# Performance work log

Measured on AMD Instinct MI355X. Metric: run time of the kernel, lower is better.

Reference implementation:

```python
import jax, jax.numpy as jnp
import numpy as np

E = 1024      # embed_dim
QH = 16       # query heads
KVH = 4       # kv heads
HD = E // QH  # head_dim = 64
KVE = HD * KVH  # 256
EPS = 1e-5
ROPE_BASE = 10000.0


def rope(x, d):
    # Faithful to the source RoPE: d == number of heads (x.shape[-2]),
    # and the 'sequence' axis of the cache is x.shape[0] (the batch dim).
    # rope(x) = x*cos + (x*sin) * neg_half(x)  (note: nonlinear in x).
    b = x.shape[0]
    theta = 1.0 / (ROPE_BASE ** (jnp.arange(0, d, 2, dtype=jnp.float32) / d))  # (d//2,)
    seq_idx = jnp.arange(b, dtype=jnp.float32)                                 # (b,)
    idx_theta = seq_idx[:, None] * theta[None, :]                              # (b, d//2)
    idx2 = jnp.concatenate([idx_theta, idx_theta], axis=-1)                    # (b, d)
    # cached shape (b,1,1,d); source permutes (0,1,3,2) -> (b,1,d,1)
    cos = jnp.cos(idx2)[:, None, :, None]  # (b,1,d,1)
    sin = jnp.sin(idx2)[:, None, :, None]
    d2 = d // 2
    # split of the LAST dim (head_dim) at d//2 == num_heads//2, as in source
    neg = jnp.concatenate([-x[..., d2:], x[..., :d2]], axis=-1)
    return x * cos + (x * sin) * neg


def setup_inputs() -> dict:
    key = jax.random.key(0)
    ks = jax.random.split(key, 12)
    b, n = 1, 2048

    def xavier(k, shape):
        fan_out, fan_in = shape
        std = (2.0 / (fan_in + fan_out)) ** 0.5
        return jax.random.normal(k, shape, dtype=jnp.float32) * std

    return {
        "query": jax.random.normal(ks[0], (b, n, E), dtype=jnp.float32),
        "key": jax.random.normal(ks[1], (b, n, E), dtype=jnp.float32),
        "value": jax.random.normal(ks[2], (b, n, E), dtype=jnp.float32),
        "Wq": xavier(ks[3], (E, E)),
        "bq": jnp.zeros((E,), jnp.float32),
        "Wk": xavier(ks[4], (KVE, E)),
        "bk": jnp.zeros((KVE,), jnp.float32),
        "Wv": xavier(ks[5], (KVE, E)),
        "bv": jnp.zeros((KVE,), jnp.float32),
        "gamma": jnp.ones((E,), jnp.float32),
        "beta": jnp.zeros((E,), jnp.float32),
    }


def reference(query, key, value, Wq, bq, Wk, bk, Wv, bv, gamma, beta):
    b, n, _ = query.shape
    q = query @ Wq.T + bq            # (b,n,E)
    k = key @ Wk.T + bk              # (b,n,KVE)
    v = value @ Wv.T + bv            # (b,n,KVE)

    q = q.reshape(b, n, QH, HD)      # b n h d
    k = k.reshape(b, n, KVH, HD)
    v = v.reshape(b, n, KVH, HD)

    q = rope(q, QH)
    k = rope(k, KVH)

    # b n h d -> b h n d
    q = jnp.transpose(q, (0, 2, 1, 3))
    k = jnp.transpose(k, (0, 2, 1, 3))
    v = jnp.transpose(v, (0, 2, 1, 3))

    scale = float(HD) ** 0.5
    q = q / scale

    g = QH // KVH
    # 'b (h g) n d -> b g h n d' : h outer, g inner
    q = q.reshape(b, KVH, g, n, HD)              # (b, h, g, n, d)
    q = jnp.transpose(q, (0, 2, 1, 3, 4))        # (b, g, h, n, d)

    sim = jnp.einsum('bghnd,bhsd->bghns', q, k)  # (b,g,h,n,s)
    attn = jax.nn.softmax(sim, axis=-1)
    out = jnp.einsum('bghns,bhsd->bghnd', attn, v)

    # 'b g h n d -> b n (h g) d'
    out = jnp.transpose(out, (0, 3, 2, 1, 4))    # (b, n, h, g, d)
    x = out.reshape(b, n, QH * HD)               # (b, n, E)

    # LayerNorm (biased variance, as in torch)
    mu = jnp.mean(x, axis=-1, keepdims=True)
    var = jnp.mean((x - mu) ** 2, axis=-1, keepdims=True)
    x = (x - mu) * jax.lax.rsqrt(var + EPS) * gamma + beta

    # NOTE: source computes out_proj(x) but returns x, so out_proj is dead code.
    return x
```

## Files before the change

### kernel.cpp

```cpp
#include <hip/hip_runtime.h>
#include <math.h>

#define EDIM   1024
#define KVEDIM 256
#define HDIM   64
#define QHEADS 16

typedef __attribute__((ext_vector_type(8))) short short8;
typedef __attribute__((ext_vector_type(4))) float f32x4;

__device__ __forceinline__ short f2b(float a) {
    unsigned ua = __builtin_bit_cast(unsigned, a);
    ua += 0x7fffu + ((ua >> 16) & 1u);
    return (short)(ua >> 16);
}
__device__ __forceinline__ unsigned cvtpk(float a, float b) {
    unsigned r;
    asm("v_cvt_pk_bf16_f32 %0, %1, %2" : "=v"(r) : "v"(a), "v"(b));
    return r;
}

__global__ __launch_bounds__(256)
void proj_gemm(const float* __restrict__ Aq, const float* __restrict__ Ak,
               const float* __restrict__ Av,
               const float* __restrict__ Wqf, const float* __restrict__ Wkf,
               const float* __restrict__ Wvf,
               const float* __restrict__ bq, const float* __restrict__ bk,
               const float* __restrict__ bv,
               short* __restrict__ Cq, short* __restrict__ Ck,
               short* __restrict__ Cv, float qscale)
{
    const int bid = blockIdx.x;
    const float* A; const float* W; const float* bias; short* C;
    int N, bm, bn; float scale;
    if (bid < 512) {
        A = Aq; W = Wqf; bias = bq; C = Cq; N = EDIM; scale = qscale;
        bm = (bid >> 4) * 64; bn = (bid & 15) * 64;
    } else if (bid < 640) {
        int i = bid - 512;
        A = Ak; W = Wkf; bias = bk; C = Ck; N = KVEDIM; scale = 1.0f;
        bm = (i >> 2) * 64; bn = (i & 3) * 64;
    } else {
        int i = bid - 640;
        A = Av; W = Wvf; bias = bv; C = Cv; N = KVEDIM; scale = 1.0f;
        bm = (i >> 2) * 64; bn = (i & 3) * 64;
    }
    const int K = EDIM;

    __shared__ short As[64 * 72];
    __shared__ short Ws[64 * 72];

    const int t = threadIdx.x, lane = t & 63, wv = t >> 6;
    const int lm = lane & 15, quad = lane >> 4;
    const int q8 = quad * 8, q4 = quad * 4;
    const int wm = (wv & 1) * 32, wn = (wv >> 1) * 32;
    const int sr = t >> 2, c0 = (t & 3) * 16;

    const f32x4 zero = {0.f, 0.f, 0.f, 0.f};
    f32x4 acc[2][2] = {{zero, zero}, {zero, zero}};

    for (int k0 = 0; k0 < K; k0 += 64) {
        __syncthreads();
        {
            const float4* ap = (const float4*)&A[(size_t)(bm + sr) * K + k0 + c0];
            float4 a0 = ap[0], a1 = ap[1], a2 = ap[2], a3 = ap[3];
            uint4 o0, o1;
            o0.x = cvtpk(a0.x, a0.y); o0.y = cvtpk(a0.z, a0.w);
            o0.z = cvtpk(a1.x, a1.y); o0.w = cvtpk(a1.z, a1.w);
            o1.x = cvtpk(a2.x, a2.y); o1.y = cvtpk(a2.z, a2.w);
            o1.z = cvtpk(a3.x, a3.y); o1.w = cvtpk(a3.z, a3.w);
            *(uint4*)&As[sr * 72 + c0]     = o0;
            *(uint4*)&As[sr * 72 + c0 + 8] = o1;
            const float4* wp = (const float4*)&W[(size_t)(bn + sr) * K + k0 + c0];
            float4 w0 = wp[0], w1 = wp[1], w2 = wp[2], w3 = wp[3];
            uint4 p0, p1;
            p0.x = cvtpk(w0.x, w0.y); p0.y = cvtpk(w0.z, w0.w);
            p0.z = cvtpk(w1.x, w1.y); p0.w = cvtpk(w1.z, w1.w);
            p1.x = cvtpk(w2.x, w2.y); p1.y = cvtpk(w2.z, w2.w);
            p1.z = cvtpk(w3.x, w3.y); p1.w = cvtpk(w3.z, w3.w);
            *(uint4*)&Ws[sr * 72 + c0]     = p0;
            *(uint4*)&Ws[sr * 72 + c0 + 8] = p1;
        }
        __syncthreads();
        #pragma unroll
        for (int ks = 0; ks < 2; ++ks) {
            short8 af[2], bfr[2];
            #pragma unroll
            for (int i = 0; i < 2; ++i)
                af[i] = *(const short8*)&As[(wm + i * 16 + lm) * 72 + ks * 32 + q8];
            #pragma unroll
            for (int j = 0; j < 2; ++j)
                bfr[j] = *(const short8*)&Ws[(wn + j * 16 + lm) * 72 + ks * 32 + q8];
            #pragma unroll
            for (int i = 0; i < 2; ++i)
                #pragma unroll
                for (int j = 0; j < 2; ++j)
                    acc[i][j] = __builtin_amdgcn_mfma_f32_16x16x32_bf16(
                        af[i], bfr[j], acc[i][j], 0, 0, 0);
        }
    }

    #pragma unroll
    for (int j = 0; j < 2; ++j) {
        float bj = bias[bn + wn + j * 16 + lm];
        #pragma unroll
        for (int i = 0; i < 2; ++i)
            #pragma unroll
            for (int r = 0; r < 4; ++r)
                C[(size_t)(bm + wm + i * 16 + q4 + r) * N + bn + wn + j * 16 + lm] =
                    f2b((acc[i][j][r] + bj) * scale);
    }
}

__global__ __launch_bounds__(256, 4)
void attn_mfma(const short* __restrict__ q, const short* __restrict__ k,
               const short* __restrict__ v, float* __restrict__ x,
               float* __restrict__ opart, float* __restrict__ lpart,
               int n, int s_len, int partial)
{
    __shared__ short Ks[2][64 * 64];
    __shared__ short Vs[2][4096];

    const int kvh = blockIdx.y;
    const int r0  = blockIdx.x * 16;
    const int t = threadIdx.x, lane = t & 63, wv = t >> 6;
    const int qh = (kvh << 2) | wv;
    const int lm = lane & 15, quad = lane >> 4, q8 = quad * 8;

    short8 qf0, qf1;
    {
        const short* qp = &q[(size_t)(r0 + lm) * EDIM + qh * HDIM];
        qf0 = *(const short8*)&qp[q8];
        qf1 = *(const short8*)&qp[32 + q8];
    }

    const f32x4 zero = {0.f, 0.f, 0.f, 0.f};
    f32x4 oacc[4] = {zero, zero, zero, zero};
    float lp = 0.f;

    const int sr  = t >> 2;
    const int scs = (t & 3) * 16;
    const int kw0 = sr * 64 + (scs ^ ((sr & 7) << 3));
    const int kw1 = sr * 64 + ((scs + 8) ^ ((sr & 7) << 3));
    const int vs4 = (t & 15) * 4;
    const int vd0 = (t >> 4) * 4;
    const int vktp = vs4 >> 5, vqd = (vs4 >> 2) & 3, vhf = (vs4 >> 4) & 1;

    const int krx  = q8 ^ ((lm & 7) << 3);
    const int krx2 = (32 + q8) ^ ((lm & 7) << 3);

    const int s_lo = (int)blockIdx.z * s_len;
    const int nt = s_len >> 6;
    const size_t kbase = (size_t)kvh * HDIM;

    uint4 kra, krb;
    uint2 vrr[4];

    {
        const uint4* ks = (const uint4*)&k[(size_t)(s_lo + sr) * KVEDIM + kbase + scs];
        kra = ks[0]; krb = ks[1];
        #pragma unroll
        for (int i = 0; i < 4; ++i)
            vrr[i] = *(const uint2*)&v[(size_t)(s_lo + vs4 + i) * KVEDIM + kbase + vd0];
    }
    {
        *(uint4*)&Ks[0][kw0] = kra;
        *(uint4*)&Ks[0][kw1] = krb;
        #pragma unroll
        for (int j = 0; j < 4; ++j) {
            const unsigned sel = (j & 1) ? 0x07060302u : 0x05040100u;
            unsigned a0 = (j < 2) ? vrr[0].x : vrr[0].y;
            unsigned a1 = (j < 2) ? vrr[1].x : vrr[1].y;
            unsigned a2 = (j < 2) ? vrr[2].x : vrr[2].y;
            unsigned a3 = (j < 2) ? vrr[3].x : vrr[3].y;
            uint2 o;
            o.x = __builtin_amdgcn_perm(a1, a0, sel);
            o.y = __builtin_amdgcn_perm(a3, a2, sel);
            const int dd = vd0 + j;
            int slot = ((dd >> 4) << 7) + (vktp << 6) + (vqd << 4) + (dd & 15);
            slot ^= (slot >> 4) & 7;
            *(uint2*)&Vs[0][slot * 8 + vhf * 4] = o;
        }
    }

    int cur = 0;
    for (int it = 0; it < nt; ++it) {
        if (it + 1 < nt) {
            const int s1 = s_lo + (it + 1) * 64;
            const uint4* ks = (const uint4*)&k[(size_t)(s1 + sr) * KVEDIM + kbase + scs];
            kra = ks[0]; krb = ks[1];
            #pragma unroll
            for (int i = 0; i < 4; ++i)
                vrr[i] = *(const uint2*)&v[(size_t)(s1 + vs4 + i) * KVEDIM + kbase + vd0];
        }

        __syncthreads();

        uint2 pa[4];
        #pragma unroll
        for (int kt = 0; kt < 4; ++kt) {
            const int krow = (kt * 16 + lm) * 64;
            short8 kf0 = *(const short8*)&Ks[cur][krow + krx];
            short8 kf1 = *(const short8*)&Ks[cur][krow + krx2];
            f32x4 s = zero;
            __builtin_amdgcn_s_setprio(1);
            s = __builtin_amdgcn_mfma_f32_16x16x32_bf16(kf0, qf0, s, 0, 0, 0);
            s = __builtin_amdgcn_mfma_f32_16x16x32_bf16(kf1, qf1, s, 0, 0, 0);
            __builtin_amdgcn_s_setprio(0);
            float p0 = exp2f(s[0]), p1 = exp2f(s[1]);
            float p2 = exp2f(s[2]), p3 = exp2f(s[3]);
            lp += (p0 + p1) + (p2 + p3);
            pa[kt].x = cvtpk(p0, p1);
            pa[kt].y = cvtpk(p2, p3);
        }

        uint4 ap0; ap0.x = pa[0].x; ap0.y = pa[0].y; ap0.z = pa[1].x; ap0.w = pa[1].y;
        uint4 ap1; ap1.x = pa[2].x; ap1.y = pa[2].y; ap1.z = pa[3].x; ap1.w = pa[3].y;
        __builtin_amdgcn_s_setprio(1);
        #pragma unroll
        for (int dt = 0; dt < 4; ++dt) {
            int sb  = (dt << 7) + (quad << 4) + lm;
            int sx0 = sb ^ ((sb >> 4) & 7);
            int sb1 = sb + 64;
            int sx1 = sb1 ^ ((sb1 >> 4) & 7);
            oacc[dt] = __builtin_amdgcn_mfma_f32_16x16x32_bf16(
                __builtin_bit_cast(short8, ap0),
                *(const short8*)&Vs[cur][sx0 * 8], oacc[dt], 0, 0, 0);
            oacc[dt] = __builtin_amdgcn_mfma_f32_16x16x32_bf16(
                __builtin_bit_cast(short8, ap1),
                *(const short8*)&Vs[cur][sx1 * 8], oacc[dt], 0, 0, 0);
        }
        __builtin_amdgcn_s_setprio(0);

        if (it + 1 < nt) {
            const int nxt = cur ^ 1;
            *(uint4*)&Ks[nxt][kw0] = kra;
            *(uint4*)&Ks[nxt][kw1] = krb;
            #pragma unroll
            for (int j = 0; j < 4; ++j) {
                const unsigned sel = (j & 1) ? 0x07060302u : 0x05040100u;
                unsigned a0 = (j < 2) ? vrr[0].x : vrr[0].y;
                unsigned a1 = (j < 2) ? vrr[1].x : vrr[1].y;
                unsigned a2 = (j < 2) ? vrr[2].x : vrr[2].y;
                unsigned a3 = (j < 2) ? vrr[3].x : vrr[3].y;
                uint2 o;
                o.x = __builtin_amdgcn_perm(a1, a0, sel);
                o.y = __builtin_amdgcn_perm(a3, a2, sel);
                const int dd = vd0 + j;
                int slot = ((dd >> 4) << 7) + (vktp << 6) + (vqd << 4) + (dd & 15);
                slot ^= (slot >> 4) & 7;
                *(uint2*)&Vs[nxt][slot * 8 + vhf * 4] = o;
            }
        }
        cur ^= 1;
    }

    float lt = lp;
    lt += __shfl_xor(lt, 16);
    lt += __shfl_xor(lt, 32);

    if (partial) {
        float* xp = opart + (size_t)blockIdx.z * n * EDIM;
        if (lane < 16)
            lpart[(size_t)blockIdx.z * n * QHEADS + (size_t)(r0 + lane) * QHEADS + qh] = lt;
        #pragma unroll
        for (int r = 0; r < 4; ++r) {
            const int row = r0 + quad * 4 + r;
            #pragma unroll
            for (int dt = 0; dt < 4; ++dt)
                xp[(size_t)row * EDIM + qh * HDIM + dt * 16 + lm] = oacc[dt][r];
        }
    } else {
        float linv[4];
        #pragma unroll
        for (int r = 0; r < 4; ++r)
            linv[r] = 1.0f / __shfl(lt, quad * 4 + r);
        #pragma unroll
        for (int r = 0; r < 4; ++r) {
            const int row = r0 + quad * 4 + r;
            #pragma unroll
            for (int dt = 0; dt < 4; ++dt)
                x[(size_t)row * EDIM + qh * HDIM + dt * 16 + lm] = oacc[dt][r] * linv[r];
        }
    }
}

__global__ __launch_bounds__(256)
void ln_kernel(float* __restrict__ x, const float* __restrict__ gamma,
               const float* __restrict__ beta,
               const float* __restrict__ opart, const float* __restrict__ lpart,
               int nsplit, int n)
{
    const int row = blockIdx.x;
    const int t = threadIdx.x;

    float4 xv;
    if (nsplit > 0) {
        const int head = t >> 4;
        float l = 0.f;
        float4 s = {0.f, 0.f, 0.f, 0.f};
        for (int z = 0; z < nsplit; ++z) {
            const float4 o = *(const float4*)&opart[(size_t)z * n * EDIM +
                                                    (size_t)row * EDIM + t * 4];
            s.x += o.x; s.y += o.y; s.z += o.z; s.w += o.w;
            l += lpart[(size_t)z * n * QHEADS + (size_t)row * QHEADS + head];
        }
        const float inv = 1.f / l;
        xv.x = s.x * inv; xv.y = s.y * inv; xv.z = s.z * inv; xv.w = s.w * inv;
    } else {
        xv = *(const float4*)&x[(size_t)row * EDIM + t * 4];
    }

    float sm  = xv.x + xv.y + xv.z + xv.w;
    float sq = xv.x * xv.x + xv.y * xv.y + xv.z * xv.z + xv.w * xv.w;
    #pragma unroll
    for (int m = 1; m < 64; m <<= 1) {
        sm += __shfl_xor(sm, m);
        sq += __shfl_xor(sq, m);
    }
    __shared__ float ws_[4], wq_[4];
    const int wave = t >> 6;
    if ((t & 63) == 0) { ws_[wave] = sm; wq_[wave] = sq; }
    __syncthreads();
    sm = ws_[0] + ws_[1] + ws_[2] + ws_[3];
    sq = wq_[0] + wq_[1] + wq_[2] + wq_[3];

    const float mu   = sm * (1.f / EDIM);
    const float var  = sq * (1.f / EDIM) - mu * mu;
    const float rstd = rsqrtf(var + 1e-5f);

    float4 g = *(const float4*)&gamma[t * 4];
    float4 b = *(const float4*)&beta[t * 4];
    float4 o;
    o.x = (xv.x - mu) * rstd * g.x + b.x;
    o.y = (xv.y - mu) * rstd * g.y + b.y;
    o.z = (xv.z - mu) * rstd * g.z + b.z;
    o.w = (xv.w - mu) * rstd * g.w + b.w;
    *(float4*)&x[(size_t)row * EDIM + t * 4] = o;
}

extern "C" void kernel_launch(void* const* d_in, const int* in_sizes, int n_in,
                              void* d_out, int out_size, void* d_ws, size_t ws_size,
                              hipStream_t stream)
{
    const float* query = (const float*)d_in[0];
    const float* key   = (const float*)d_in[1];
    const float* value = (const float*)d_in[2];
    const float* Wq    = (const float*)d_in[3];
    const float* bq    = (const float*)d_in[4];
    const float* Wk    = (const float*)d_in[5];
    const float* bk    = (const float*)d_in[6];
    const float* Wv    = (const float*)d_in[7];
    const float* bv    = (const float*)d_in[8];
    const float* gamma = (const float*)d_in[9];
    const float* beta  = (const float*)d_in[10];
    float* out = (float*)d_out;

    const int n = in_sizes[0] / EDIM;

    short* qb  = (short*)d_ws;
    short* kb  = qb + (size_t)n * EDIM;
    short* vb  = kb + (size_t)n * KVEDIM;
    short* ws_end = vb + (size_t)n * KVEDIM;

    const size_t base_bytes = (size_t)((char*)ws_end - (char*)d_ws);
    int nsplit = 0;
    {
        const int cand = 2;
        size_t need = base_bytes +
                      (size_t)cand * ((size_t)n * EDIM + (size_t)n * QHEADS) * sizeof(float);
        if ((n % (64 * cand)) == 0 && need <= ws_size) nsplit = cand;
    }
    float* opart = (float*)ws_end;
    float* lpart = opart + (size_t)(nsplit > 0 ? nsplit : 1) * n * EDIM;

    const float qscale = 0.125f * 1.44269504088896f;

    proj_gemm<<<dim3(768), 256, 0, stream>>>(
        query, key, value, Wq, Wk, Wv, bq, bk, bv, qb, kb, vb, qscale);

    const int zdim  = (nsplit > 0) ? nsplit : 1;
    const int s_len = n / zdim;
    attn_mfma<<<dim3(n / 16, 4, zdim), 256, 0, stream>>>(
        qb, kb, vb, out, opart, lpart, n, s_len, nsplit > 0 ? 1 : 0);

    ln_kernel<<<dim3(n), 256, 0, stream>>>(out, gamma, beta, opart, lpart, nsplit, n);
}
```

Before: 165.5 us.

## Store V transposed in projection and read K/V fragments directly from global

The V projection epilogue now writes V transposed (head-dim major, sequence contiguous) as packed bf16. The attention kernel drops its double-buffered LDS staging of K and V, the barriers and the setprio hints, and loads MFMA operand fragments straight from global memory, relying on cache reuse across the four waves that share a KV head. This removes LDS traffic and synchronisation, but each wave now issues its own scattered global loads with no software prefetch, so load latency sits directly on the MFMA path. The occupancy hint on launch bounds is also removed.

New measurement: 289.9 us. 1.75x slower.

```diff
diff --git a/kernel.cpp b/kernel.cpp
--- a/kernel.cpp
+++ b/kernel.cpp
@@ -28,21 +28,21 @@
                const float* __restrict__ bq, const float* __restrict__ bk,
                const float* __restrict__ bv,
                short* __restrict__ Cq, short* __restrict__ Ck,
-               short* __restrict__ Cv, float qscale)
+               short* __restrict__ Cv, float qscale, int n)
 {
     const int bid = blockIdx.x;
     const float* A; const float* W; const float* bias; short* C;
-    int N, bm, bn; float scale;
+    int N, bm, bn; float scale; int vtrans;
     if (bid < 512) {
-        A = Aq; W = Wqf; bias = bq; C = Cq; N = EDIM; scale = qscale;
+        A = Aq; W = Wqf; bias = bq; C = Cq; N = EDIM; scale = qscale; vtrans = 0;
         bm = (bid >> 4) * 64; bn = (bid & 15) * 64;
     } else if (bid < 640) {
         int i = bid - 512;
-        A = Ak; W = Wkf; bias = bk; C = Ck; N = KVEDIM; scale = 1.0f;
+        A = Ak; W = Wkf; bias = bk; C = Ck; N = KVEDIM; scale = 1.0f; vtrans = 0;
         bm = (i >> 2) * 64; bn = (i & 3) * 64;
     } else {
         int i = bid - 640;
-        A = Av; W = Wvf; bias = bv; C = Cv; N = KVEDIM; scale = 1.0f;
+        A = Av; W = Wvf; bias = bv; C = Cv; N = KVEDIM; scale = 1.0f; vtrans = 1;
         bm = (i >> 2) * 64; bn = (i & 3) * 64;
     }
     const int K = EDIM;
@@ -100,27 +100,39 @@
         }
     }
 
-    #pragma unroll
-    for (int j = 0; j < 2; ++j) {
-        float bj = bias[bn + wn + j * 16 + lm];
-        #pragma unroll
-        for (int i = 0; i < 2; ++i)
-            #pragma unroll
-            for (int r = 0; r < 4; ++r)
-                C[(size_t)(bm + wm + i * 16 + q4 + r) * N + bn + wn + j * 16 + lm] =
-                    f2b((acc[i][j][r] + bj) * scale);
-    }
-}
-
-__global__ __launch_bounds__(256, 4)
+    if (!vtrans) {
+        #pragma unroll
+        for (int j = 0; j < 2; ++j) {
+            float bj = bias[bn + wn + j * 16 + lm];
+            #pragma unroll
+            for (int i = 0; i < 2; ++i)
+                #pragma unroll
+                for (int r = 0; r < 4; ++r)
+                    C[(size_t)(bm + wm + i * 16 + q4 + r) * N + bn + wn + j * 16 + lm] =
+                        f2b((acc[i][j][r] + bj) * scale);
+        }
+    } else {
+        #pragma unroll
+        for (int j = 0; j < 2; ++j) {
+            float bj = bias[bn + wn + j * 16 + lm];
+            const size_t drow = (size_t)(bn + wn + j * 16 + lm) * n;
+            #pragma unroll
+            for (int i = 0; i < 2; ++i) {
+                uint2 o;
+                o.x = cvtpk(acc[i][j][0] + bj, acc[i][j][1] + bj);
+                o.y = cvtpk(acc[i][j][2] + bj, acc[i][j][3] + bj);
+                *(uint2*)&C[drow + bm + wm + i * 16 + q4] = o;
+            }
+        }
+    }
+}
+
+__global__ __launch_bounds__(256)
 void attn_mfma(const short* __restrict__ q, const short* __restrict__ k,
-               const short* __restrict__ v, float* __restrict__ x,
+               const short* __restrict__ vt, float* __restrict__ x,
                float* __restrict__ opart, float* __restrict__ lpart,
                int n, int s_len, int partial)
 {
-    __shared__ short Ks[2][64 * 64];
-    __shared__ short Vs[2][4096];
-
     const int kvh = blockIdx.y;
     const int r0  = blockIdx.x * 16;
     const int t = threadIdx.x, lane = t & 63, wv = t >> 6;
@@ -138,75 +150,24 @@
     f32x4 oacc[4] = {zero, zero, zero, zero};
     float lp = 0.f;
 
-    const int sr  = t >> 2;
-    const int scs = (t & 3) * 16;
-    const int kw0 = sr * 64 + (scs ^ ((sr & 7) << 3));
-    const int kw1 = sr * 64 + ((scs + 8) ^ ((sr & 7) << 3));
-    const int vs4 = (t & 15) * 4;
-    const int vd0 = (t >> 4) * 4;
-    const int vktp = vs4 >> 5, vqd = (vs4 >> 2) & 3, vhf = (vs4 >> 4) & 1;
-
-    const int krx  = q8 ^ ((lm & 7) << 3);
-    const int krx2 = (32 + q8) ^ ((lm & 7) << 3);
-
     const int s_lo = (int)blockIdx.z * s_len;
     const int nt = s_len >> 6;
-    const size_t kbase = (size_t)kvh * HDIM;
-
-    uint4 kra, krb;
-    uint2 vrr[4];
-
-    {
-        const uint4* ks = (const uint4*)&k[(size_t)(s_lo + sr) * KVEDIM + kbase + scs];
-        kra = ks[0]; krb = ks[1];
-        #pragma unroll
-        for (int i = 0; i < 4; ++i)
-            vrr[i] = *(const uint2*)&v[(size_t)(s_lo + vs4 + i) * KVEDIM + kbase + vd0];
-    }
-    {
-        *(uint4*)&Ks[0][kw0] = kra;
-        *(uint4*)&Ks[0][kw1] = krb;
-        #pragma unroll
-        for (int j = 0; j < 4; ++j) {
-            const unsigned sel = (j & 1) ? 0x07060302u : 0x05040100u;
-            unsigned a0 = (j < 2) ? vrr[0].x : vrr[0].y;
-            unsigned a1 = (j < 2) ? vrr[1].x : vrr[1].y;
-            unsigned a2 = (j < 2) ? vrr[2].x : vrr[2].y;
-            unsigned a3 = (j < 2) ? vrr[3].x : vrr[3].y;
-            uint2 o;
-            o.x = __builtin_amdgcn_perm(a1, a0, sel);
-            o.y = __builtin_amdgcn_perm(a3, a2, sel);
-            const int dd = vd0 + j;
-            int slot = ((dd >> 4) << 7) + (vktp << 6) + (vqd << 4) + (dd & 15);
-            slot ^= (slot >> 4) & 7;
-            *(uint2*)&Vs[0][slot * 8 + vhf * 4] = o;
-        }
-    }
-
-    int cur = 0;
+    const short* kb = k + (size_t)kvh * HDIM;
+    const short* vb = vt + (size_t)(kvh * HDIM) * n;
+
     for (int it = 0; it < nt; ++it) {
-        if (it + 1 < nt) {
-            const int s1 = s_lo + (it + 1) * 64;
-            const uint4* ks = (const uint4*)&k[(size_t)(s1 + sr) * KVEDIM + kbase + scs];
-            kra = ks[0]; krb = ks[1];
-            #pragma unroll
-            for (int i = 0; i < 4; ++i)
-                vrr[i] = *(const uint2*)&v[(size_t)(s1 + vs4 + i) * KVEDIM + kbase + vd0];
-        }
-
-        __syncthreads();
+        const int s0 = s_lo + it * 64;
 
         uint2 pa[4];
+        const short* kp = kb + (size_t)s0 * KVEDIM;
         #pragma unroll
         for (int kt = 0; kt < 4; ++kt) {
-            const int krow = (kt * 16 + lm) * 64;
-            short8 kf0 = *(const short8*)&Ks[cur][krow + krx];
-            short8 kf1 = *(const short8*)&Ks[cur][krow + krx2];
+            const short* kr = kp + (size_t)(kt * 16 + lm) * KVEDIM;
+            short8 kf0 = *(const short8*)&kr[q8];
+            short8 kf1 = *(const short8*)&kr[32 + q8];
             f32x4 s = zero;
-            __builtin_amdgcn_s_setprio(1);
             s = __builtin_amdgcn_mfma_f32_16x16x32_bf16(kf0, qf0, s, 0, 0, 0);
             s = __builtin_amdgcn_mfma_f32_16x16x32_bf16(kf1, qf1, s, 0, 0, 0);
-            __builtin_amdgcn_s_setprio(0);
             float p0 = exp2f(s[0]), p1 = exp2f(s[1]);
             float p2 = exp2f(s[2]), p3 = exp2f(s[3]);
             lp += (p0 + p1) + (p2 + p3);
@@ -216,43 +177,22 @@
 
         uint4 ap0; ap0.x = pa[0].x; ap0.y = pa[0].y; ap0.z = pa[1].x; ap0.w = pa[1].y;
         uint4 ap1; ap1.x = pa[2].x; ap1.y = pa[2].y; ap1.z = pa[3].x; ap1.w = pa[3].y;
-        __builtin_amdgcn_s_setprio(1);
         #pragma unroll
         for (int dt = 0; dt < 4; ++dt) {
-            int sb  = (dt << 7) + (quad << 4) + lm;
-            int sx0 = sb ^ ((sb >> 4) & 7);
-            int sb1 = sb + 64;
-            int sx1 = sb1 ^ ((sb1 >> 4) & 7);
+            const short* vr = vb + (size_t)(dt * 16 + lm) * n + s0 + quad * 4;
+            uint2 lo0 = *(const uint2*)&vr[0];
+            uint2 hi0 = *(const uint2*)&vr[16];
+            uint2 lo1 = *(const uint2*)&vr[32];
+            uint2 hi1 = *(const uint2*)&vr[48];
+            uint4 b0; b0.x = lo0.x; b0.y = lo0.y; b0.z = hi0.x; b0.w = hi0.y;
+            uint4 b1; b1.x = lo1.x; b1.y = lo1.y; b1.z = hi1.x; b1.w = hi1.y;
             oacc[dt] = __builtin_amdgcn_mfma_f32_16x16x32_bf16(
                 __builtin_bit_cast(short8, ap0),
-                *(const short8*)&Vs[cur][sx0 * 8], oacc[dt], 0, 0, 0);
+                __builtin_bit_cast(short8, b0), oacc[dt], 0, 0, 0);
             oacc[dt] = __builtin_amdgcn_mfma_f32_16x16x32_bf16(
                 __builtin_bit_cast(short8, ap1),
-                *(const short8*)&Vs[cur][sx1 * 8], oacc[dt], 0, 0, 0);
-        }
-        __builtin_amdgcn_s_setprio(0);
-
-        if (it + 1 < nt) {
-            const int nxt = cur ^ 1;
-            *(uint4*)&Ks[nxt][kw0] = kra;
-            *(uint4*)&Ks[nxt][kw1] = krb;
-            #pragma unroll
-            for (int j = 0; j < 4; ++j) {
-                const unsigned sel = (j & 1) ? 0x07060302u : 0x05040100u;
-                unsigned a0 = (j < 2) ? vrr[0].x : vrr[0].y;
-                unsigned a1 = (j < 2) ? vrr[1].x : vrr[1].y;
-                unsigned a2 = (j < 2) ? vrr[2].x : vrr[2].y;
-                unsigned a3 = (j < 2) ? vrr[3].x : vrr[3].y;
-                uint2 o;
-                o.x = __builtin_amdgcn_perm(a1, a0, sel);
-                o.y = __builtin_amdgcn_perm(a3, a2, sel);
-                const int dd = vd0 + j;
-                int slot = ((dd >> 4) << 7) + (vktp << 6) + (vqd << 4) + (dd & 15);
-                slot ^= (slot >> 4) & 7;
-                *(uint2*)&Vs[nxt][slot * 8 + vhf * 4] = o;
-            }
-        }
-        cur ^= 1;
+                __builtin_bit_cast(short8, b1), oacc[dt], 0, 0, 0);
+        }
     }
 
     float lt = lp;
@@ -360,8 +300,8 @@
 
     short* qb  = (short*)d_ws;
     short* kb  = qb + (size_t)n * EDIM;
-    short* vb  = kb + (size_t)n * KVEDIM;
-    short* ws_end = vb + (size_t)n * KVEDIM;
+    short* vtb = kb + (size_t)n * KVEDIM;
+    short* ws_end = vtb + (size_t)KVEDIM * n;
 
     const size_t base_bytes = (size_t)((char*)ws_end - (char*)d_ws);
     int nsplit = 0;
@@ -377,12 +317,12 @@
     const float qscale = 0.125f * 1.44269504088896f;
 
     proj_gemm<<<dim3(768), 256, 0, stream>>>(
-        query, key, value, Wq, Wk, Wv, bq, bk, bv, qb, kb, vb, qscale);
+        query, key, value, Wq, Wk, Wv, bq, bk, bv, qb, kb, vtb, qscale, n);
 
     const int zdim  = (nsplit > 0) ? nsplit : 1;
     const int s_len = n / zdim;
     attn_mfma<<<dim3(n / 16, 4, zdim), 256, 0, stream>>>(
-        qb, kb, vb, out, opart, lpart, n, s_len, nsplit > 0 ? 1 : 0);
+        qb, kb, vtb, out, opart, lpart, n, s_len, nsplit > 0 ? 1 : 0);
 
     ln_kernel<<<dim3(n), 256, 0, stream>>>(out, gamma, beta, opart, lpart, nsplit, n);
 }
```
